# Kernel tuning notes

Hardware: AMD Instinct MI355X
Metric: run time of the kernel (lower is better)

Reference implementation:

```python
import jax, jax.numpy as jnp
import numpy as np

B, H, S, D = 4, 16, 2048, 128

def setup_inputs() -> dict:
    key = jax.random.key(0)
    kq, kk, kv = jax.random.split(key, 3)
    query = jax.random.normal(kq, (B, H, S, D), dtype=jnp.float32)
    k = jax.random.normal(kk, (B, H, S, D), dtype=jnp.float32)
    v = jax.random.normal(kv, (B, H, S, D), dtype=jnp.float32)
    # causal mask: True = masked (not attended), broadcastable to (B,H,S,S)
    mask = jnp.triu(jnp.ones((S, S), dtype=bool), k=1)[None, None, :, :]
    return {"query": query, "key": k, "value": v, "mask": mask}

def reference(query, key, value, mask):
    d_k = query.shape[-1]
    scale = 1.0 / np.sqrt(d_k).astype(np.float32)
    # scores: (B,H,Sq,Sk)
    scores = jnp.einsum('bhqd,bhkd->bhqk', query, key) * scale
    scores = jnp.where(mask, -jnp.inf, scores)
    attention_weights = jax.nn.softmax(scores, axis=-1)
    output = jnp.einsum('bhqk,bhkd->bhqd', attention_weights, value)
    return output, attention_weights
```

## Files before the change

kernel.cpp:

```cpp
#include <hip/hip_runtime.h>
#include <hip/hip_bf16.h>

#define B_ 4
#define H_ 16
#define S_ 2048
#define D_ 128

typedef unsigned short u16;
typedef unsigned int u32;

typedef __attribute__((ext_vector_type(8))) short bf16x8;
typedef __attribute__((ext_vector_type(4))) float f32x4;
typedef __attribute__((ext_vector_type(4))) unsigned short u16x4;

__device__ __forceinline__ float bf2f(u16 x) {
    return __uint_as_float(((u32)x) << 16);
}

__device__ __forceinline__ u16 f2bf(float f) {
    u32 u = __float_as_uint(f);
    u32 lsb = (u >> 16) & 1u;
    u += 0x7fffu + lsb;
    return (u16)(u >> 16);
}

#define LBAR() do {                                            \
    asm volatile("s_waitcnt lgkmcnt(0)" ::: "memory");         \
    __builtin_amdgcn_s_barrier();                              \
} while (0)

__global__ void detect_dtype_kernel(const u32* __restrict__ q, int* __restrict__ flag) {
    __shared__ int cnt;
    if (threadIdx.x == 0) cnt = 0;
    __syncthreads();
    int c = 0;
    for (int i = threadIdx.x; i < 4096; i += 256) {
        float lo = bf2f((u16)(q[i] & 0xffffu));
        if (!(fabsf(lo) <= 64.0f)) c++;
    }
    atomicAdd(&cnt, c);
    __syncthreads();
    if (threadIdx.x == 0) *flag = (cnt > 256) ? 1 : 0;
}

__global__ __launch_bounds__(256) void attn_bf16_kernel(
    const u16* __restrict__ Q, const u16* __restrict__ K, const u16* __restrict__ V,
    u16* __restrict__ Out, u16* __restrict__ W, const int* __restrict__ flag)
{
    if (*flag != 0) return;

    __shared__ float qs[D_];
    __shared__ float sc[S_];
    __shared__ float red[8];
    __shared__ float ot[512];

    const int tid = threadIdx.x;
    for (int idx = blockIdx.x; idx < B_ * H_ * S_; idx += (int)gridDim.x) {
        const int q   = idx & (S_ - 1);
        const int bh  = idx >> 11;
        const size_t rowQ = (size_t)idx * D_;
        const u16* Kb = K + (size_t)bh * S_ * D_;
        const u16* Vb = V + (size_t)bh * S_ * D_;
        const int nk = q + 1;
        const float scale = 0.08838834764831845f;

        if (tid < D_) qs[tid] = bf2f(Q[rowQ + tid]) * scale;
        __syncthreads();

        float lmax = -1e30f;
        for (int k = tid; k < nk; k += 256) {
            const uint4* K4 = reinterpret_cast<const uint4*>(Kb + (size_t)k * D_);
            float acc = 0.f;
            #pragma unroll
            for (int c = 0; c < D_ / 8; ++c) {
                uint4 u = K4[c];
                const int d = c * 8;
                acc += qs[d + 0] * bf2f((u16)(u.x & 0xffffu));
                acc += qs[d + 1] * bf2f((u16)(u.x >> 16));
                acc += qs[d + 2] * bf2f((u16)(u.y & 0xffffu));
                acc += qs[d + 3] * bf2f((u16)(u.y >> 16));
                acc += qs[d + 4] * bf2f((u16)(u.z & 0xffffu));
                acc += qs[d + 5] * bf2f((u16)(u.z >> 16));
                acc += qs[d + 6] * bf2f((u16)(u.w & 0xffffu));
                acc += qs[d + 7] * bf2f((u16)(u.w >> 16));
            }
            sc[k] = acc;
            lmax = fmaxf(lmax, acc);
        }

        #pragma unroll
        for (int off = 32; off > 0; off >>= 1)
            lmax = fmaxf(lmax, __shfl_down(lmax, off, 64));
        if ((tid & 63) == 0) red[tid >> 6] = lmax;
        __syncthreads();
        const float mx = fmaxf(fmaxf(red[0], red[1]), fmaxf(red[2], red[3]));

        float lsum = 0.f;
        for (int k = tid; k < nk; k += 256) {
            float e = __expf(sc[k] - mx);
            sc[k] = e;
            lsum += e;
        }
        #pragma unroll
        for (int off = 32; off > 0; off >>= 1)
            lsum += __shfl_down(lsum, off, 64);
        if ((tid & 63) == 0) red[4 + (tid >> 6)] = lsum;
        __syncthreads();
        const float rsum = 1.0f / (red[4] + red[5] + red[6] + red[7]);

        u32* Wrow2 = reinterpret_cast<u32*>(W + (size_t)idx * S_);
        for (int k2 = tid; k2 < S_ / 2; k2 += 256) {
            const int k0 = 2 * k2, k1 = 2 * k2 + 1;
            float w0 = (k0 < nk) ? sc[k0] * rsum : 0.f;
            float w1 = (k1 < nk) ? sc[k1] * rsum : 0.f;
            if (k0 < nk) sc[k0] = w0;
            if (k1 < nk) sc[k1] = w1;
            Wrow2[k2] = (u32)f2bf(w0) | ((u32)f2bf(w1) << 16);
        }
        __syncthreads();

        const int d2   = tid & 63;
        const int part = tid >> 6;
        const u32* V2 = reinterpret_cast<const u32*>(Vb);
        float a0 = 0.f, a1 = 0.f;
        for (int k = part; k < nk; k += 4) {
            const u32 u = V2[(size_t)k * (D_ / 2) + d2];
            const float w = sc[k];
            a0 += w * bf2f((u16)(u & 0xffffu));
            a1 += w * bf2f((u16)(u >> 16));
        }
        ot[part * D_ + 2 * d2]     = a0;
        ot[part * D_ + 2 * d2 + 1] = a1;
        __syncthreads();

        if (tid < D_) {
            const float o = ot[tid] + ot[D_ + tid] + ot[2 * D_ + tid] + ot[3 * D_ + tid];
            Out[rowQ + tid] = f2bf(o);
        }
        __syncthreads();
    }
}

__global__ __launch_bounds__(256) void split_qk_kernel(
    const float* __restrict__ Q, const float* __restrict__ K,
    u16* __restrict__ Qh, u16* __restrict__ Ql,
    u16* __restrict__ Kh, u16* __restrict__ Kl,
    const int* __restrict__ flag)
{
    if (*flag != 1) return;
    const float scale = 0.08838834764831845f;
    const int N4 = (B_ * H_ * S_ * D_) / 4;
    const float4* Q4 = reinterpret_cast<const float4*>(Q);
    const float4* K4 = reinterpret_cast<const float4*>(K);
    for (int g = blockIdx.x * 256 + threadIdx.x; g < N4; g += 2048 * 256) {
        {
            float4 v = Q4[g];
            float s0 = v.x * scale, s1 = v.y * scale, s2 = v.z * scale, s3 = v.w * scale;
            u16 h0 = f2bf(s0), h1 = f2bf(s1), h2 = f2bf(s2), h3 = f2bf(s3);
            u16x4 hv = {h0, h1, h2, h3};
            u16x4 lv = {f2bf(s0 - bf2f(h0)), f2bf(s1 - bf2f(h1)),
                        f2bf(s2 - bf2f(h2)), f2bf(s3 - bf2f(h3))};
            *reinterpret_cast<u16x4*>(&Qh[(size_t)4 * g]) = hv;
            *reinterpret_cast<u16x4*>(&Ql[(size_t)4 * g]) = lv;
        }
        {
            float4 v = K4[g];
            u16 h0 = f2bf(v.x), h1 = f2bf(v.y), h2 = f2bf(v.z), h3 = f2bf(v.w);
            u16x4 hv = {h0, h1, h2, h3};
            u16x4 lv = {f2bf(v.x - bf2f(h0)), f2bf(v.y - bf2f(h1)),
                        f2bf(v.z - bf2f(h2)), f2bf(v.w - bf2f(h3))};
            *reinterpret_cast<u16x4*>(&Kh[(size_t)4 * g]) = hv;
            *reinterpret_cast<u16x4*>(&Kl[(size_t)4 * g]) = lv;
        }
    }
}

__global__ __launch_bounds__(256) void transpose_v_kernel(
    const float* __restrict__ V, u16* __restrict__ VT, const int* __restrict__ flag)
{
    if (*flag != 1) return;
    __shared__ float ts[64 * 130];
    const int tid = threadIdx.x;
    const int bh = blockIdx.x >> 5;
    const int kt = blockIdx.x & 31;
    const int k0 = kt * 64;
    const float4* V4 = reinterpret_cast<const float4*>(V + ((size_t)bh * S_ + k0) * D_);
    #pragma unroll
    for (int it = 0; it < 8; ++it) {
        int g = tid + 256 * it;
        int r = g >> 5, c4 = g & 31;
        float4 v = V4[g];
        ts[r * 130 + 4 * c4 + 0] = v.x;
        ts[r * 130 + 4 * c4 + 1] = v.y;
        ts[r * 130 + 4 * c4 + 2] = v.z;
        ts[r * 130 + 4 * c4 + 3] = v.w;
    }
    __syncthreads();
    const int d = tid >> 1, kh2 = tid & 1;
    u16* dst = VT + (size_t)bh * (D_ * S_) + (size_t)d * S_ + k0 + 32 * kh2;
    #pragma unroll
    for (int jj = 0; jj < 4; ++jj) {
        bf16x8 o;
        #pragma unroll
        for (int j = 0; j < 8; ++j) {
            int k = 32 * kh2 + 8 * jj + j;
            o[j] = (short)f2bf(ts[k * 130 + d]);
        }
        *reinterpret_cast<bf16x8*>(&dst[8 * jj]) = o;
    }
}

#define ESTR 68

__global__ __launch_bounds__(256, 2) void attn_mfma_kernel(
    const u16* __restrict__ Qh, const u16* __restrict__ Ql,
    const u16* __restrict__ Kh, const u16* __restrict__ Kl,
    const u16* __restrict__ VT,
    float* __restrict__ Out, float* __restrict__ W, const int* __restrict__ flag)
{
    if (*flag != 1) return;

    __shared__ __align__(16) short kh_s[64 * 128];
    __shared__ __align__(16) short kl_s[64 * 128];
    __shared__ __align__(16) short vt_s[128 * 64];
    __shared__ __align__(16) float e_s[32 * ESTR];
    __shared__ float red2[2][32];
    __shared__ float rinv_s[32];

    const int tid = threadIdx.x;
    const int w   = tid >> 6;
    const int l   = tid & 63;
    const int l15 = l & 15;
    const int l4  = l >> 4;
    const int fq  = w >> 1;
    const int fk  = w & 1;

    const int nwg = (int)gridDim.x;
    const int bid = blockIdx.x;
    const int wk  = (bid & 7) * (nwg >> 3) + (bid >> 3);
    const int bh  = wk >> 6;
    const int qt  = 63 - (wk & 63);
    const int q0  = qt << 5;
    const int nkt = (q0 + 95) >> 6;

    const u16* QhB = Qh + ((size_t)bh * S_ + q0) * D_;
    const u16* QlB = Ql + ((size_t)bh * S_ + q0) * D_;
    const u16* KhB = Kh + (size_t)bh * S_ * D_;
    const u16* KlB = Kl + (size_t)bh * S_ * D_;
    const u16* VTB = VT + (size_t)bh * (size_t)D_ * S_;
    float* Ob = Out + ((size_t)bh * S_ + q0) * D_;
    float* Wb = W + ((size_t)bh * S_ + q0) * (size_t)S_;

    const int qrow = 16 * fq + l15;
    const int col0 = 8 * l4;

    bf16x8 aQH[4], aQL[4];
    #pragma unroll
    for (int ks = 0; ks < 4; ++ks) {
        aQH[ks] = *reinterpret_cast<const bf16x8*>(&QhB[(size_t)qrow * D_ + 32 * ks + col0]);
        aQL[ks] = *reinterpret_cast<const bf16x8*>(&QlB[(size_t)qrow * D_ + 32 * ks + col0]);
    }

    float rs[4] = {0.f, 0.f, 0.f, 0.f};

    {
        bf16x8 rkh[4];
        #pragma unroll
        for (int it = 0; it < 4; ++it) {
            int g = tid + 256 * it;
            rkh[it] = *reinterpret_cast<const bf16x8*>(&KhB[(size_t)(g >> 4) * D_ + 8 * (g & 15)]);
        }

        for (int kt = 0; kt < nkt; ++kt) {
            const int k0 = kt << 6;
            #pragma unroll
            for (int it = 0; it < 4; ++it) {
                int g = tid + 256 * it;
                int r = g >> 4, ch = g & 15;
                int li = r * 128 + ((8 * ch) ^ ((r & 7) << 3));
                *reinterpret_cast<bf16x8*>(&kh_s[li]) = rkh[it];
            }
            LBAR();

            if (kt + 1 < nkt) {
                const int kn = k0 + 64;
                #pragma unroll
                for (int it = 0; it < 4; ++it) {
                    int g = tid + 256 * it;
                    rkh[it] = *reinterpret_cast<const bf16x8*>(&KhB[(size_t)(kn + (g >> 4)) * D_ + 8 * (g & 15)]);
                }
            }

            f32x4 acc2[2];
            acc2[0] = {0.f, 0.f, 0.f, 0.f};
            acc2[1] = {0.f, 0.f, 0.f, 0.f};
            __builtin_amdgcn_s_setprio(1);
            #pragma unroll
            for (int nb = 0; nb < 2; ++nb) {
                const int krow = 32 * fk + 16 * nb + l15;
                const int kx   = (krow & 7) << 3;
                #pragma unroll
                for (int ks = 0; ks < 4; ++ks) {
                    int ca = 32 * ks + col0;
                    bf16x8 bH = *reinterpret_cast<const bf16x8*>(&kh_s[krow * 128 + (ca ^ kx)]);
                    acc2[nb] = __builtin_amdgcn_mfma_f32_16x16x32_bf16(aQH[ks], bH, acc2[nb], 0, 0, 0);
                }
            }
            __builtin_amdgcn_s_setprio(0);

            #pragma unroll
            for (int nb = 0; nb < 2; ++nb) {
                #pragma unroll
                for (int i = 0; i < 4; ++i) {
                    int row = 16 * fq + 4 * l4 + i;
                    int col = 32 * fk + 16 * nb + l15;
                    if (k0 + col <= q0 + row) rs[i] += __expf(acc2[nb][i]);
                }
            }
            LBAR();
        }
    }

    #pragma unroll
    for (int i = 0; i < 4; ++i) {
        float v = rs[i];
        v += __shfl_xor(v, 1, 64);
        v += __shfl_xor(v, 2, 64);
        v += __shfl_xor(v, 4, 64);
        v += __shfl_xor(v, 8, 64);
        if (l15 == 0) red2[fk][16 * fq + 4 * l4 + i] = v;
    }
    __syncthreads();
    if (tid < 32) rinv_s[tid] = 1.0f / (red2[0][tid] + red2[1][tid]);
    __syncthreads();

    float rinvr[4];
    #pragma unroll
    for (int i = 0; i < 4; ++i) rinvr[i] = rinv_s[16 * fq + 4 * l4 + i];

    f32x4 oacc[4];
    #pragma unroll
    for (int nb = 0; nb < 4; ++nb) { oacc[nb] = {0.f, 0.f, 0.f, 0.f}; }

    {
        bf16x8 rkh[4], rkl[4], rvt[4];
        #pragma unroll
        for (int it = 0; it < 4; ++it) {
            int g = tid + 256 * it;
            rkh[it] = *reinterpret_cast<const bf16x8*>(&KhB[(size_t)(g >> 4) * D_ + 8 * (g & 15)]);
            rkl[it] = *reinterpret_cast<const bf16x8*>(&KlB[(size_t)(g >> 4) * D_ + 8 * (g & 15)]);
            rvt[it] = *reinterpret_cast<const bf16x8*>(&VTB[(size_t)(g >> 3) * S_ + 8 * (g & 7)]);
        }

        for (int kt = 0; kt < nkt; ++kt) {
            const int k0 = kt << 6;
            #pragma unroll
            for (int it = 0; it < 4; ++it) {
                int g = tid + 256 * it;
                int r = g >> 4, ch = g & 15;
                int li = r * 128 + ((8 * ch) ^ ((r & 7) << 3));
                *reinterpret_cast<bf16x8*>(&kh_s[li]) = rkh[it];
                *reinterpret_cast<bf16x8*>(&kl_s[li]) = rkl[it];
                int d = g >> 3, c8 = g & 7;
                *reinterpret_cast<bf16x8*>(&vt_s[d * 64 + 8 * (c8 ^ (d & 7))]) = rvt[it];
            }
            LBAR();

            if (kt + 1 < nkt) {
                const int kn = k0 + 64;
                #pragma unroll
                for (int it = 0; it < 4; ++it) {
                    int g = tid + 256 * it;
                    rkh[it] = *reinterpret_cast<const bf16x8*>(&KhB[(size_t)(kn + (g >> 4)) * D_ + 8 * (g & 15)]);
                    rkl[it] = *reinterpret_cast<const bf16x8*>(&KlB[(size_t)(kn + (g >> 4)) * D_ + 8 * (g & 15)]);
                    rvt[it] = *reinterpret_cast<const bf16x8*>(&VTB[(size_t)(g >> 3) * S_ + kn + 8 * (g & 7)]);
                }
            }

            f32x4 acc2[2];
            acc2[0] = {0.f, 0.f, 0.f, 0.f};
            acc2[1] = {0.f, 0.f, 0.f, 0.f};
            __builtin_amdgcn_s_setprio(1);
            #pragma unroll
            for (int nb = 0; nb < 2; ++nb) {
                const int krow = 32 * fk + 16 * nb + l15;
                const int kx   = (krow & 7) << 3;
                #pragma unroll
                for (int ks = 0; ks < 4; ++ks) {
                    int ca = 32 * ks + col0;
                    bf16x8 bH = *reinterpret_cast<const bf16x8*>(&kh_s[krow * 128 + (ca ^ kx)]);
                    bf16x8 bL = *reinterpret_cast<const bf16x8*>(&kl_s[krow * 128 + (ca ^ kx)]);
                    acc2[nb] = __builtin_amdgcn_mfma_f32_16x16x32_bf16(aQH[ks], bH, acc2[nb], 0, 0, 0);
                    acc2[nb] = __builtin_amdgcn_mfma_f32_16x16x32_bf16(aQH[ks], bL, acc2[nb], 0, 0, 0);
                    acc2[nb] = __builtin_amdgcn_mfma_f32_16x16x32_bf16(aQL[ks], bH, acc2[nb], 0, 0, 0);
                }
            }
            __builtin_amdgcn_s_setprio(0);

            #pragma unroll
            for (int nb = 0; nb < 2; ++nb) {
                #pragma unroll
                for (int i = 0; i < 4; ++i) {
                    int row = 16 * fq + 4 * l4 + i;
                    int col = 32 * fk + 16 * nb + l15;
                    float e = 0.f;
                    if (k0 + col <= q0 + row) e = __expf(acc2[nb][i]) * rinvr[i];
                    e_s[row * ESTR + col] = e;
                }
            }
            LBAR();

            #pragma unroll
            for (int t = 0; t < 2; ++t) {
                int idx = tid + 256 * t;
                int row = idx >> 4, c4 = idx & 15;
                f32x4 wv = *reinterpret_cast<const f32x4*>(&e_s[row * ESTR + 4 * c4]);
                __builtin_nontemporal_store(wv,
                    reinterpret_cast<f32x4*>(Wb + (size_t)row * S_ + k0 + 4 * c4));
            }

            #pragma unroll
            for (int ks2 = 0; ks2 < 2; ++ks2) {
                bf16x8 aP;
                {
                    const float* pr = &e_s[(16 * fq + l15) * ESTR + 32 * ks2 + col0];
                    float4 p0 = *reinterpret_cast<const float4*>(pr);
                    float4 p1 = *reinterpret_cast<const float4*>(pr + 4);
                    aP[0] = (short)f2bf(p0.x); aP[1] = (short)f2bf(p0.y);
                    aP[2] = (short)f2bf(p0.z); aP[3] = (short)f2bf(p0.w);
                    aP[4] = (short)f2bf(p1.x); aP[5] = (short)f2bf(p1.y);
                    aP[6] = (short)f2bf(p1.z); aP[7] = (short)f2bf(p1.w);
                }
                __builtin_amdgcn_s_setprio(1);
                #pragma unroll
                for (int nb = 0; nb < 4; ++nb) {
                    int dcol = 64 * fk + 16 * nb + l15;
                    bf16x8 bV = *reinterpret_cast<const bf16x8*>(
                        &vt_s[dcol * 64 + 8 * ((4 * ks2 + l4) ^ (dcol & 7))]);
                    oacc[nb] = __builtin_amdgcn_mfma_f32_16x16x32_bf16(aP, bV, oacc[nb], 0, 0, 0);
                }
                __builtin_amdgcn_s_setprio(0);
            }
            LBAR();
        }
    }

    #pragma unroll
    for (int nb = 0; nb < 4; ++nb) {
        #pragma unroll
        for (int i = 0; i < 4; ++i) {
            int row = 16 * fq + 4 * l4 + i;
            int col = 64 * fk + 16 * nb + l15;
            __builtin_nontemporal_store(oacc[nb][i], &Ob[(size_t)row * D_ + col]);
        }
    }

    {
        const int kend4 = nkt << 4;
        f32x4* W4 = reinterpret_cast<f32x4*>(Wb);
        const f32x4 z4 = {0.f, 0.f, 0.f, 0.f};
        const int zc = 512 - kend4;
        for (int g = tid; g < 32 * zc; g += 256) {
            const int row = g / zc;
            const int c4  = kend4 + (g - row * zc);
            __builtin_nontemporal_store(z4, &W4[(size_t)row * 512 + c4]);
        }
    }
}

#define BQ 32
#define BK 64
#define LSTR 33
#define FESTR 68

__device__ __forceinline__ void dot4(float& a, const float4& x, const float4& y) {
    a = fmaf(x.x, y.x, a); a = fmaf(x.y, y.y, a);
    a = fmaf(x.z, y.z, a); a = fmaf(x.w, y.w, a);
}
__device__ __forceinline__ void fma4(float4& a, float s, const float4& b) {
    a.x = fmaf(s, b.x, a.x); a.y = fmaf(s, b.y, a.y);
    a.z = fmaf(s, b.z, a.z); a.w = fmaf(s, b.w, a.w);
}

__global__ __launch_bounds__(256) void attn_f32_tiled(
    const float* __restrict__ Q, const float* __restrict__ K, const float* __restrict__ V,
    float* __restrict__ Out, float* __restrict__ W, const int* __restrict__ flag)
{
    if (*flag != 1) return;

    __shared__ float4 qs4[BQ * LSTR];
    __shared__ float4 kv4[BK * LSTR];
    __shared__ __align__(16) float e_s[BQ * FESTR];
    __shared__ float rsum_s[BQ];
    __shared__ float rinv_s[BQ];

    const int tid  = threadIdx.x;
    const int bidx = blockIdx.x;
    const int bh   = bidx >> 6;
    const int qt   = 63 - (bidx & 63);
    const int q0   = qt << 5;
    const int nkt  = ((q0 + BQ - 1) >> 6) + 1;
    const float scale = 0.08838834764831845f;

    const float* Kb = K + (size_t)bh * (S_ * D_);
    const float* Vb = V + (size_t)bh * (S_ * D_);
    const float* Qb = Q + ((size_t)bh * S_ + q0) * D_;
    float* Ob = Out + ((size_t)bh * S_ + q0) * D_;
    float* Wb = W + ((size_t)bh * S_ + q0) * (size_t)S_;

    const int rgq = tid >> 4;
    const int cgq = tid & 15;
    const int rg = tid >> 4;
    const int cg = tid & 15;

    {
        const float4* Qg = reinterpret_cast<const float4*>(Qb);
        #pragma unroll
        for (int t = 0; t < 4; ++t) {
            const int g = tid + 256 * t;
            qs4[(g >> 5) * LSTR + (g & 31)] = Qg[g];
        }
        const float4* Kg = reinterpret_cast<const float4*>(Kb);
        #pragma unroll
        for (int t = 0; t < 8; ++t) {
            const int g = tid + 256 * t;
            kv4[(g >> 5) * LSTR + (g & 31)] = Kg[g];
        }
    }
    __syncthreads();

    float4 o4[2][2] = {};
    float rsf[2] = {0.f, 0.f};

    for (int kt = 0; kt < nkt; ++kt) {
        const int k0 = kt << 6;
        const bool more = (kt + 1 < nkt);

        float4 vreg[8];
        {
            const float4* Vg = reinterpret_cast<const float4*>(Vb) + (size_t)k0 * 32;
            #pragma unroll
            for (int t = 0; t < 8; ++t) vreg[t] = Vg[tid + 256 * t];
        }

        float acc[2][4] = {};
        {
            const int qb0 = (rgq * 2 + 0) * LSTR;
            const int qb1 = (rgq * 2 + 1) * LSTR;
            const int kb0 = (cgq +  0) * LSTR;
            const int kb1 = (cgq + 16) * LSTR;
            const int kb2 = (cgq + 32) * LSTR;
            const int kb3 = (cgq + 48) * LSTR;
            #pragma unroll 4
            for (int d4 = 0; d4 < 32; ++d4) {
                const float4 qv0 = qs4[qb0 + d4];
                const float4 qv1 = qs4[qb1 + d4];
                const float4 kv0 = kv4[kb0 + d4];
                const float4 kv1 = kv4[kb1 + d4];
                const float4 kv2 = kv4[kb2 + d4];
                const float4 kv3 = kv4[kb3 + d4];
                dot4(acc[0][0], qv0, kv0); dot4(acc[0][1], qv0, kv1);
                dot4(acc[0][2], qv0, kv2); dot4(acc[0][3], qv0, kv3);
                dot4(acc[1][0], qv1, kv0); dot4(acc[1][1], qv1, kv1);
                dot4(acc[1][2], qv1, kv2); dot4(acc[1][3], qv1, kv3);
            }
        }

        #pragma unroll
        for (int i = 0; i < 2; ++i) {
            const int r  = rgq * 2 + i;
            const int qg = q0 + r;
            float* Wrow = Wb + (size_t)r * S_ + k0;
            #pragma unroll
            for (int j = 0; j < 4; ++j) {
                const int kc = cgq + 16 * j;
                const float e = (k0 + kc <= qg) ? __expf(acc[i][j] * scale) : 0.0f;
                rsf[i] += e;
                e_s[r * FESTR + kc] = e;
                Wrow[kc] = e;
            }
        }
        __syncthreads();

        #pragma unroll
        for (int t = 0; t < 8; ++t) {
            const int g = tid + 256 * t;
            kv4[(g >> 5) * LSTR + (g & 31)] = vreg[t];
        }
        float4 kreg[8];
        if (more) {
            const float4* Kg = reinterpret_cast<const float4*>(Kb) + (size_t)(k0 + BK) * 32;
            #pragma unroll
            for (int t = 0; t < 8; ++t) kreg[t] = Kg[tid + 256 * t];
        }
        __syncthreads();

        {
            const int eb0 = (rg * 2 + 0) * FESTR;
            const int eb1 = (rg * 2 + 1) * FESTR;
            #pragma unroll 2
            for (int kk = 0; kk < BK; kk += 4) {
                const float4 e0 = *reinterpret_cast<const float4*>(&e_s[eb0 + kk]);
                const float4 e1 = *reinterpret_cast<const float4*>(&e_s[eb1 + kk]);
                const float ea[4] = {e0.x, e0.y, e0.z, e0.w};
                const float eb[4] = {e1.x, e1.y, e1.z, e1.w};
                #pragma unroll
                for (int t = 0; t < 4; ++t) {
                    const float4 v0 = kv4[(kk + t) * LSTR + cg];
                    const float4 v1 = kv4[(kk + t) * LSTR + 16 + cg];
                    fma4(o4[0][0], ea[t], v0);
                    fma4(o4[0][1], ea[t], v1);
                    fma4(o4[1][0], eb[t], v0);
                    fma4(o4[1][1], eb[t], v1);
                }
            }
        }

        if (more) {
            __syncthreads();
            #pragma unroll
            for (int t = 0; t < 8; ++t) {
                const int g = tid + 256 * t;
                kv4[(g >> 5) * LSTR + (g & 31)] = kreg[t];
            }
            __syncthreads();
        }
    }

    #pragma unroll
    for (int i = 0; i < 2; ++i) {
        float v = rsf[i];
        v += __shfl_xor(v, 8, 64);
        v += __shfl_xor(v, 4, 64);
        v += __shfl_xor(v, 2, 64);
        v += __shfl_xor(v, 1, 64);
        if (cgq == 0) rsum_s[rgq * 2 + i] = v;
    }
    __syncthreads();
    if (tid < BQ) rinv_s[tid] = 1.0f / rsum_s[tid];
    __syncthreads();

    #pragma unroll
    for (int i = 0; i < 2; ++i) {
        const int r = rg * 2 + i;
        const float inv = rinv_s[r];
        float4 a = o4[i][0];
        a.x *= inv; a.y *= inv; a.z *= inv; a.w *= inv;
        float4 b = o4[i][1];
        b.x *= inv; b.y *= inv; b.z *= inv; b.w *= inv;
        float4* Orow = reinterpret_cast<float4*>(Ob + (size_t)r * D_);
        Orow[cg]      = a;
        Orow[16 + cg] = b;
    }

    {
        const int kend = nkt << 6;
        float4* W4 = reinterpret_cast<float4*>(Wb);
        for (int g = tid; g < BQ * (S_ / 4); g += 256) {
            const int row = g >> 9;
            const int c4  = g & 511;
            const size_t off = (size_t)row * (S_ / 4) + c4;
            if ((c4 << 2) < kend) {
                float4 wv = W4[off];
                const float inv = rinv_s[row];
                wv.x *= inv; wv.y *= inv; wv.z *= inv; wv.w *= inv;
                W4[off] = wv;
            } else {
                W4[off] = make_float4(0.f, 0.f, 0.f, 0.f);
            }
        }
    }
}

extern "C" void kernel_launch(void* const* d_in, const int* in_sizes, int n_in,
                              void* d_out, int out_size, void* d_ws, size_t ws_size,
                              hipStream_t stream) {
    int* flag = (int*)d_ws;

    detect_dtype_kernel<<<dim3(1), dim3(256), 0, stream>>>((const u32*)d_in[0], flag);

    {
        const u16* Q = (const u16*)d_in[0];
        const u16* K = (const u16*)d_in[1];
        const u16* V = (const u16*)d_in[2];
        u16* Out = (u16*)d_out;
        u16* Wp  = Out + (size_t)B_ * H_ * S_ * D_;
        attn_bf16_kernel<<<dim3(2048), dim3(256), 0, stream>>>(Q, K, V, Out, Wp, flag);
    }

    const size_t PLSZ = (size_t)B_ * H_ * S_ * D_;
    const size_t NEED = 256 + 5 * PLSZ * sizeof(u16);
    float* OutF = (float*)d_out;
    float* WF   = OutF + PLSZ;

    if (ws_size >= NEED) {
        u16* base = (u16*)((char*)d_ws + 256);
        u16* Qh = base;
        u16* Ql = Qh + PLSZ;
        u16* Kh = Ql + PLSZ;
        u16* Kl = Kh + PLSZ;
        u16* VTp = Kl + PLSZ;
        split_qk_kernel<<<dim3(2048), dim3(256), 0, stream>>>(
            (const float*)d_in[0], (const float*)d_in[1], Qh, Ql, Kh, Kl, flag);
        transpose_v_kernel<<<dim3(2048), dim3(256), 0, stream>>>(
            (const float*)d_in[2], VTp, flag);
        attn_mfma_kernel<<<dim3(B_ * H_ * (S_ / 32)), dim3(256), 0, stream>>>(
            Qh, Ql, Kh, Kl, VTp, OutF, WF, flag);
    } else {
        attn_f32_tiled<<<dim3(B_ * H_ * (S_ / 32)), dim3(256), 0, stream>>>(
            (const float*)d_in[0], (const float*)d_in[1], (const float*)d_in[2],
            OutF, WF, flag);
    }
}
```

Measured before the change: 1.646 ms.

## Merge prep kernels, store probabilities as bf16 in LDS, raise occupancy

Fuses the Q/K split kernel and the V transpose into one launch with block-index dispatch, removing one kernel launch and its tail. The attention kernel now keeps softmax probabilities in LDS as bf16 instead of fp32. That roughly halves the probability tile's LDS footprint and lets the MFMA operand be loaded directly without per-element conversion. Launch bounds are raised to 3 blocks per CU to increase occupancy. Side effect: the attention weights written out are now bf16-rounded values widened back to fp32, which loses precision in the W output.

```diff
diff --git a/kernel.cpp b/kernel.cpp
--- a/kernel.cpp
+++ b/kernel.cpp
@@ -141,78 +141,77 @@
     }
 }
 
-__global__ __launch_bounds__(256) void split_qk_kernel(
-    const float* __restrict__ Q, const float* __restrict__ K,
+__global__ __launch_bounds__(256) void prep_kernel(
+    const float* __restrict__ Q, const float* __restrict__ K, const float* __restrict__ V,
     u16* __restrict__ Qh, u16* __restrict__ Ql,
     u16* __restrict__ Kh, u16* __restrict__ Kl,
-    const int* __restrict__ flag)
-{
-    if (*flag != 1) return;
-    const float scale = 0.08838834764831845f;
-    const int N4 = (B_ * H_ * S_ * D_) / 4;
-    const float4* Q4 = reinterpret_cast<const float4*>(Q);
-    const float4* K4 = reinterpret_cast<const float4*>(K);
-    for (int g = blockIdx.x * 256 + threadIdx.x; g < N4; g += 2048 * 256) {
-        {
-            float4 v = Q4[g];
-            float s0 = v.x * scale, s1 = v.y * scale, s2 = v.z * scale, s3 = v.w * scale;
-            u16 h0 = f2bf(s0), h1 = f2bf(s1), h2 = f2bf(s2), h3 = f2bf(s3);
-            u16x4 hv = {h0, h1, h2, h3};
-            u16x4 lv = {f2bf(s0 - bf2f(h0)), f2bf(s1 - bf2f(h1)),
-                        f2bf(s2 - bf2f(h2)), f2bf(s3 - bf2f(h3))};
-            *reinterpret_cast<u16x4*>(&Qh[(size_t)4 * g]) = hv;
-            *reinterpret_cast<u16x4*>(&Ql[(size_t)4 * g]) = lv;
-        }
-        {
-            float4 v = K4[g];
-            u16 h0 = f2bf(v.x), h1 = f2bf(v.y), h2 = f2bf(v.z), h3 = f2bf(v.w);
-            u16x4 hv = {h0, h1, h2, h3};
-            u16x4 lv = {f2bf(v.x - bf2f(h0)), f2bf(v.y - bf2f(h1)),
-                        f2bf(v.z - bf2f(h2)), f2bf(v.w - bf2f(h3))};
-            *reinterpret_cast<u16x4*>(&Kh[(size_t)4 * g]) = hv;
-            *reinterpret_cast<u16x4*>(&Kl[(size_t)4 * g]) = lv;
-        }
-    }
-}
-
-__global__ __launch_bounds__(256) void transpose_v_kernel(
-    const float* __restrict__ V, u16* __restrict__ VT, const int* __restrict__ flag)
+    u16* __restrict__ VT, const int* __restrict__ flag)
 {
     if (*flag != 1) return;
     __shared__ float ts[64 * 130];
     const int tid = threadIdx.x;
-    const int bh = blockIdx.x >> 5;
-    const int kt = blockIdx.x & 31;
-    const int k0 = kt * 64;
-    const float4* V4 = reinterpret_cast<const float4*>(V + ((size_t)bh * S_ + k0) * D_);
-    #pragma unroll
-    for (int it = 0; it < 8; ++it) {
-        int g = tid + 256 * it;
-        int r = g >> 5, c4 = g & 31;
-        float4 v = V4[g];
-        ts[r * 130 + 4 * c4 + 0] = v.x;
-        ts[r * 130 + 4 * c4 + 1] = v.y;
-        ts[r * 130 + 4 * c4 + 2] = v.z;
-        ts[r * 130 + 4 * c4 + 3] = v.w;
-    }
-    __syncthreads();
-    const int d = tid >> 1, kh2 = tid & 1;
-    u16* dst = VT + (size_t)bh * (D_ * S_) + (size_t)d * S_ + k0 + 32 * kh2;
-    #pragma unroll
-    for (int jj = 0; jj < 4; ++jj) {
-        bf16x8 o;
-        #pragma unroll
-        for (int j = 0; j < 8; ++j) {
-            int k = 32 * kh2 + 8 * jj + j;
-            o[j] = (short)f2bf(ts[k * 130 + d]);
-        }
-        *reinterpret_cast<bf16x8*>(&dst[8 * jj]) = o;
-    }
-}
-
-#define ESTR 68
-
-__global__ __launch_bounds__(256, 2) void attn_mfma_kernel(
+
+    if (blockIdx.x < 2048) {
+        const float scale = 0.08838834764831845f;
+        const int N4 = (B_ * H_ * S_ * D_) / 4;
+        const float4* Q4 = reinterpret_cast<const float4*>(Q);
+        const float4* K4 = reinterpret_cast<const float4*>(K);
+        for (int g = blockIdx.x * 256 + tid; g < N4; g += 2048 * 256) {
+            {
+                float4 v = Q4[g];
+                float s0 = v.x * scale, s1 = v.y * scale, s2 = v.z * scale, s3 = v.w * scale;
+                u16 h0 = f2bf(s0), h1 = f2bf(s1), h2 = f2bf(s2), h3 = f2bf(s3);
+                u16x4 hv = {h0, h1, h2, h3};
+                u16x4 lv = {f2bf(s0 - bf2f(h0)), f2bf(s1 - bf2f(h1)),
+                            f2bf(s2 - bf2f(h2)), f2bf(s3 - bf2f(h3))};
+                *reinterpret_cast<u16x4*>(&Qh[(size_t)4 * g]) = hv;
+                *reinterpret_cast<u16x4*>(&Ql[(size_t)4 * g]) = lv;
+            }
+            {
+                float4 v = K4[g];
+                u16 h0 = f2bf(v.x), h1 = f2bf(v.y), h2 = f2bf(v.z), h3 = f2bf(v.w);
+                u16x4 hv = {h0, h1, h2, h3};
+                u16x4 lv = {f2bf(v.x - bf2f(h0)), f2bf(v.y - bf2f(h1)),
+                            f2bf(v.z - bf2f(h2)), f2bf(v.w - bf2f(h3))};
+                *reinterpret_cast<u16x4*>(&Kh[(size_t)4 * g]) = hv;
+                *reinterpret_cast<u16x4*>(&Kl[(size_t)4 * g]) = lv;
+            }
+        }
+    } else {
+        const int bid = blockIdx.x - 2048;
+        const int bh = bid >> 5;
+        const int kt = bid & 31;
+        const int k0 = kt * 64;
+        const float4* V4 = reinterpret_cast<const float4*>(V + ((size_t)bh * S_ + k0) * D_);
+        #pragma unroll
+        for (int it = 0; it < 8; ++it) {
+            int g = tid + 256 * it;
+            int r = g >> 5, c4 = g & 31;
+            float4 v = V4[g];
+            ts[r * 130 + 4 * c4 + 0] = v.x;
+            ts[r * 130 + 4 * c4 + 1] = v.y;
+            ts[r * 130 + 4 * c4 + 2] = v.z;
+            ts[r * 130 + 4 * c4 + 3] = v.w;
+        }
+        __syncthreads();
+        const int d = tid >> 1, kh2 = tid & 1;
+        u16* dst = VT + (size_t)bh * (D_ * S_) + (size_t)d * S_ + k0 + 32 * kh2;
+        #pragma unroll
+        for (int jj = 0; jj < 4; ++jj) {
+            bf16x8 o;
+            #pragma unroll
+            for (int j = 0; j < 8; ++j) {
+                int k = 32 * kh2 + 8 * jj + j;
+                o[j] = (short)f2bf(ts[k * 130 + d]);
+            }
+            *reinterpret_cast<bf16x8*>(&dst[8 * jj]) = o;
+        }
+    }
+}
+
+#define ESTRE 72
+
+__global__ __launch_bounds__(256, 3) void attn_mfma_kernel(
     const u16* __restrict__ Qh, const u16* __restrict__ Ql,
     const u16* __restrict__ Kh, const u16* __restrict__ Kl,
     const u16* __restrict__ VT,
@@ -223,7 +222,7 @@
     __shared__ __align__(16) short kh_s[64 * 128];
     __shared__ __align__(16) short kl_s[64 * 128];
     __shared__ __align__(16) short vt_s[128 * 64];
-    __shared__ __align__(16) float e_s[32 * ESTR];
+    __shared__ __align__(16) u16 ep_s[32 * ESTRE];
     __shared__ float red2[2][32];
     __shared__ float rinv_s[32];
 
@@ -405,7 +404,7 @@
                     int col = 32 * fk + 16 * nb + l15;
                     float e = 0.f;
                     if (k0 + col <= q0 + row) e = __expf(acc2[nb][i]) * rinvr[i];
-                    e_s[row * ESTR + col] = e;
+                    ep_s[row * ESTRE + col] = f2bf(e);
                 }
             }
             LBAR();
@@ -414,23 +413,16 @@
             for (int t = 0; t < 2; ++t) {
                 int idx = tid + 256 * t;
                 int row = idx >> 4, c4 = idx & 15;
-                f32x4 wv = *reinterpret_cast<const f32x4*>(&e_s[row * ESTR + 4 * c4]);
+                u16x4 pv = *reinterpret_cast<const u16x4*>(&ep_s[row * ESTRE + 4 * c4]);
+                f32x4 wv = { bf2f(pv.x), bf2f(pv.y), bf2f(pv.z), bf2f(pv.w) };
                 __builtin_nontemporal_store(wv,
                     reinterpret_cast<f32x4*>(Wb + (size_t)row * S_ + k0 + 4 * c4));
             }
 
             #pragma unroll
             for (int ks2 = 0; ks2 < 2; ++ks2) {
-                bf16x8 aP;
-                {
-                    const float* pr = &e_s[(16 * fq + l15) * ESTR + 32 * ks2 + col0];
-                    float4 p0 = *reinterpret_cast<const float4*>(pr);
-                    float4 p1 = *reinterpret_cast<const float4*>(pr + 4);
-                    aP[0] = (short)f2bf(p0.x); aP[1] = (short)f2bf(p0.y);
-                    aP[2] = (short)f2bf(p0.z); aP[3] = (short)f2bf(p0.w);
-                    aP[4] = (short)f2bf(p1.x); aP[5] = (short)f2bf(p1.y);
-                    aP[6] = (short)f2bf(p1.z); aP[7] = (short)f2bf(p1.w);
-                }
+                bf16x8 aP = *reinterpret_cast<const bf16x8*>(
+                    &ep_s[(16 * fq + l15) * ESTRE + 32 * ks2 + col0]);
                 __builtin_amdgcn_s_setprio(1);
                 #pragma unroll
                 for (int nb = 0; nb < 4; ++nb) {
@@ -700,10 +692,9 @@
         u16* Kh = Ql + PLSZ;
         u16* Kl = Kh + PLSZ;
         u16* VTp = Kl + PLSZ;
-        split_qk_kernel<<<dim3(2048), dim3(256), 0, stream>>>(
-            (const float*)d_in[0], (const float*)d_in[1], Qh, Ql, Kh, Kl, flag);
-        transpose_v_kernel<<<dim3(2048), dim3(256), 0, stream>>>(
-            (const float*)d_in[2], VTp, flag);
+        prep_kernel<<<dim3(4096), dim3(256), 0, stream>>>(
+            (const float*)d_in[0], (const float*)d_in[1], (const float*)d_in[2],
+            Qh, Ql, Kh, Kl, VTp, flag);
         attn_mfma_kernel<<<dim3(B_ * H_ * (S_ / 32)), dim3(256), 0, stream>>>(
             Qh, Ql, Kh, Kl, VTp, OutF, WF, flag);
     } else {
```

Result: slower. 1.739 ms (+5.6%).
